# Optimization experiments

Measured on AMD Instinct MI355X. Metric: run time of the kernel, lower is better.

The kernel has to match this reference:

```python
import jax, jax.numpy as jnp
import numpy as np

N_NODES = 50000
N_EDGES = 300000
HEADS = 2
OUT_CH = 128
BN_EPS = 1e-5
NEG_SLOPE = 0.2


def _batchnorm(x, g, b):
    # training-mode BatchNorm1d: biased batch statistics
    mean = x.mean(axis=0)
    var = x.var(axis=0)
    return (x - mean) * jax.lax.rsqrt(var + BN_EPS) * g + b


def _gatv2(x, src, dst, edge_attr, Wl, bl, Wr, br, We, att, bias, concat):
    # PyG GATv2Conv, share_weights=False, aggr='add'
    n = x.shape[0]
    xl = (x @ Wl + bl).reshape(n, HEADS, OUT_CH)  # source messages
    xr = (x @ Wr + br).reshape(n, HEADS, OUT_CH)  # destination term
    ee = (edge_attr @ We).reshape(-1, HEADS, OUT_CH)
    s = jax.nn.leaky_relu(xl[src] + xr[dst] + ee, NEG_SLOPE)  # [E,H,C]
    alpha = jnp.einsum('ehc,hc->eh', s, att)  # [E,H]
    # segment softmax over edges grouped by destination node
    m = jax.ops.segment_max(alpha, dst, num_segments=n)
    a = jnp.exp(alpha - m[dst])
    den = jax.ops.segment_sum(a, dst, num_segments=n)
    a = a / (den[dst] + 1e-16)
    out = jax.ops.segment_sum(xl[src] * a[:, :, None], dst, num_segments=n)  # [N,H,C]
    out = out.reshape(n, HEADS * OUT_CH) if concat else out.mean(axis=1)
    return out + bias


def setup_inputs() -> dict:
    key = jax.random.key(0)
    ks = jax.random.split(key, 16)
    d = {}
    d['h'] = jax.random.normal(ks[0], (N_NODES, 5), jnp.float32)
    d['edge_index'] = jax.random.randint(ks[1], (2, N_EDGES), 0, N_NODES, jnp.int64)
    d['edge_weight'] = jax.random.uniform(ks[2], (N_EDGES, 1), jnp.float32)
    d['bn0_g'] = jnp.ones((5,), jnp.float32)
    d['bn0_b'] = jnp.zeros((5,), jnp.float32)
    d['bn1_g'] = jnp.ones((256,), jnp.float32)
    d['bn1_b'] = jnp.zeros((256,), jnp.float32)
    def lin(k, fan_in, fan_out):
        return jax.random.normal(k, (fan_in, fan_out), jnp.float32) * (1.0 / np.sqrt(fan_in))
    # conv1: in=5 -> heads*out=256, concat=True
    d['c1_Wl'] = lin(ks[3], 5, 256); d['c1_bl'] = jnp.zeros((256,), jnp.float32)
    d['c1_Wr'] = lin(ks[4], 5, 256); d['c1_br'] = jnp.zeros((256,), jnp.float32)
    d['c1_We'] = lin(ks[5], 1, 256)
    d['c1_att'] = jax.random.normal(ks[6], (HEADS, OUT_CH), jnp.float32) * 0.1
    d['c1_bias'] = jnp.zeros((256,), jnp.float32)
    # mu: in=256 -> 128, concat=False
    d['mu_Wl'] = lin(ks[7], 256, 256); d['mu_bl'] = jnp.zeros((256,), jnp.float32)
    d['mu_Wr'] = lin(ks[8], 256, 256); d['mu_br'] = jnp.zeros((256,), jnp.float32)
    d['mu_We'] = lin(ks[9], 1, 256)
    d['mu_att'] = jax.random.normal(ks[10], (HEADS, OUT_CH), jnp.float32) * 0.1
    d['mu_bias'] = jnp.zeros((128,), jnp.float32)
    # log_std: same shapes as mu
    d['ls_Wl'] = lin(ks[11], 256, 256); d['ls_bl'] = jnp.zeros((256,), jnp.float32)
    d['ls_Wr'] = lin(ks[12], 256, 256); d['ls_br'] = jnp.zeros((256,), jnp.float32)
    d['ls_We'] = lin(ks[13], 1, 256)
    d['ls_att'] = jax.random.normal(ks[14], (HEADS, OUT_CH), jnp.float32) * 0.1
    d['ls_bias'] = jnp.zeros((128,), jnp.float32)
    return d


def reference(h, edge_index, edge_weight, bn0_g, bn0_b, bn1_g, bn1_b,
              c1_Wl, c1_bl, c1_Wr, c1_br, c1_We, c1_att, c1_bias,
              mu_Wl, mu_bl, mu_Wr, mu_br, mu_We, mu_att, mu_bias,
              ls_Wl, ls_bl, ls_Wr, ls_br, ls_We, ls_att, ls_bias):
    src, dst = edge_index[0], edge_index[1]
    x = _batchnorm(h, bn0_g, bn0_b)
    x = _gatv2(x, src, dst, edge_weight, c1_Wl, c1_bl, c1_Wr, c1_br, c1_We, c1_att, c1_bias, concat=True)
    x = jax.nn.relu(_batchnorm(x, bn1_g, bn1_b))
    # dropout identity (eval / deterministic)
    mu = _gatv2(x, src, dst, edge_weight, mu_Wl, mu_bl, mu_Wr, mu_br, mu_We, mu_att, mu_bias, concat=False)
    log_std = _gatv2(x, src, dst, edge_weight, ls_Wl, ls_bl, ls_Wr, ls_br, ls_We, ls_att, ls_bias, concat=False)
    return (mu, log_std)
```

## Files before the change

### kernel.cpp

```cpp
#include <hip/hip_runtime.h>
#include <math.h>

#define N_NODES 50000
#define N_EDGES 300000
#define BN_EPS 1e-5f
#define NEG_SLOPE 0.2f

#define RB_COUNT 3128
#define SCAN_TILES 49
#define BN1_BLOCKS 523

typedef short bf8v __attribute__((ext_vector_type(8)));
typedef float f4v __attribute__((ext_vector_type(4)));
typedef float f2v __attribute__((ext_vector_type(2)));

__device__ inline unsigned short f2bf(float f) {
    union { float f; unsigned u; } c; c.f = f;
    unsigned r = c.u + 0x7fffu + ((c.u >> 16) & 1u);
    return (unsigned short)(r >> 16);
}

__device__ inline f2v bfpair(unsigned u) {
    union { unsigned u; float f; } lo, hi;
    lo.u = u << 16;
    hi.u = u & 0xffff0000u;
    f2v r; r.x = lo.f; r.y = hi.f;
    return r;
}

__device__ inline void async_copy16(void* lds, const void* g) {
    __builtin_amdgcn_global_load_lds(
        (const __attribute__((address_space(1))) unsigned int*)g,
        (__attribute__((address_space(3))) unsigned int*)lds, 16, 0, 0);
}

__global__ void bn0_reduce(const float* __restrict__ h, float* __restrict__ acc ) {
    __shared__ float lds[4][10];
    int tid = threadIdx.x;
    int lane = tid & 63, wave = tid >> 6;
    float ls[5] = {0,0,0,0,0}, lq[5] = {0,0,0,0,0};
    for (int r = blockIdx.x * 256 + tid; r < N_NODES; r += 128 * 256) {
        #pragma unroll
        for (int k = 0; k < 5; k++) {
            float v = h[r*5 + k];
            ls[k] += v; lq[k] += v*v;
        }
    }
    #pragma unroll
    for (int k = 0; k < 5; k++) {
        #pragma unroll
        for (int m = 1; m <= 32; m <<= 1) {
            ls[k] += __shfl_xor(ls[k], m, 64);
            lq[k] += __shfl_xor(lq[k], m, 64);
        }
    }
    if (lane == 0) {
        #pragma unroll
        for (int k = 0; k < 5; k++) { lds[wave][k] = ls[k]; lds[wave][5+k] = lq[k]; }
    }
    __syncthreads();
    if (tid < 10) {
        float s = lds[0][tid] + lds[1][tid] + lds[2][tid] + lds[3][tid];
        atomicAdd(&acc[tid], s);
    }
}

__global__ void bn0_finalize(const float* __restrict__ acc, const float* __restrict__ g,
                             const float* __restrict__ b, float* __restrict__ ss) {
    int tid = threadIdx.x;
    if (tid < 5) {
        float mean = acc[tid] * (1.f / N_NODES);
        float var  = acc[5 + tid] * (1.f / N_NODES) - mean*mean;
        float sc = g[tid] * rsqrtf(var + BN_EPS);
        ss[tid]     = sc;
        ss[5 + tid] = b[tid] - mean * sc;
    }
}

__global__ void edge_count(const int* __restrict__ dst, int* __restrict__ count) {
    int e = blockIdx.x * blockDim.x + threadIdx.x;
    if (e < N_EDGES) atomicAdd(&count[dst[e]], 1);
}

__global__ void local_scan(const int* __restrict__ count, int* __restrict__ offsets,
                           int* __restrict__ tileSum) {
    __shared__ int lds[1024];
    int tid = threadIdx.x;
    int i = blockIdx.x * 1024 + tid;
    int v = (i < N_NODES) ? count[i] : 0;
    lds[tid] = v;
    __syncthreads();
    #pragma unroll
    for (int off = 1; off < 1024; off <<= 1) {
        int t = (tid >= off) ? lds[tid - off] : 0;
        __syncthreads();
        lds[tid] += t;
        __syncthreads();
    }
    if (i < N_NODES) offsets[i] = lds[tid] - v;
    if (tid == 1023) tileSum[blockIdx.x] = lds[1023];
}

__global__ void tile_scan(const int* __restrict__ tileSum, int* __restrict__ tilePrefix,
                          int* __restrict__ offsets) {
    int lane = threadIdx.x;
    int v = (lane < SCAN_TILES) ? tileSum[lane] : 0;
    int inc = v;
    #pragma unroll
    for (int off = 1; off < 64; off <<= 1) {
        int t = __shfl_up(inc, off, 64);
        if (lane >= off) inc += t;
    }
    int excl = inc - v;
    if (lane < SCAN_TILES) tilePrefix[lane] = excl;
    if (lane == SCAN_TILES - 1) offsets[N_NODES] = inc;
}

__global__ void add_prefix(int* __restrict__ offsets, const int* __restrict__ tilePrefix,
                           int* __restrict__ cursor) {
    int i = blockIdx.x * 1024 + threadIdx.x;
    if (i < N_NODES) {
        int o = offsets[i] + tilePrefix[blockIdx.x];
        offsets[i] = o;
        cursor[i] = o;
    }
}

__global__ void edge_scatter(const int* __restrict__ dst, const int* __restrict__ src,
                             const float* __restrict__ ew, int* __restrict__ cursor,
                             int* __restrict__ srcp, float* __restrict__ ewp) {
    int e = blockIdx.x * blockDim.x + threadIdx.x;
    if (e < N_EDGES) {
        int pos = atomicAdd(&cursor[dst[e]], 1);
        srcp[pos] = src[e];
        ewp[pos] = ew[e];
    }
}

__global__ void gemm_k5(const float* __restrict__ h, const float* __restrict__ ss,
                        const float* __restrict__ Wl, const float* __restrict__ bl,
                        const float* __restrict__ Wr, const float* __restrict__ br,
                        unsigned short* __restrict__ xl, unsigned short* __restrict__ xr) {
    int n = blockIdx.x;
    int c = threadIdx.x * 2;
    float a[5];
    #pragma unroll
    for (int k = 0; k < 5; k++) a[k] = h[n*5 + k] * ss[k] + ss[5 + k];
    float l0 = bl[c], l1 = bl[c+1], r0 = br[c], r1 = br[c+1];
    #pragma unroll
    for (int k = 0; k < 5; k++) {
        l0 += a[k] * Wl[k*256 + c];
        l1 += a[k] * Wl[k*256 + c + 1];
        r0 += a[k] * Wr[k*256 + c];
        r1 += a[k] * Wr[k*256 + c + 1];
    }
    unsigned lp = (unsigned)f2bf(l0) | ((unsigned)f2bf(l1) << 16);
    unsigned rp = (unsigned)f2bf(r0) | ((unsigned)f2bf(r1) << 16);
    *reinterpret_cast<unsigned*>(xl + (size_t)n*256 + c) = lp;
    *reinterpret_cast<unsigned*>(xr + (size_t)n*256 + c) = rp;
}

__global__ void pack_x_bn(const float* __restrict__ x, const float* __restrict__ ss1,
                          unsigned short* __restrict__ ap) {
    int t = blockIdx.x * 256 + threadIdx.x;
    int lane = t & 63;
    int kc = (t >> 6) & 7;
    int rb = t >> 9;
    int row = rb * 16 + (lane & 15);
    int k0 = kc * 32 + (lane >> 4) * 8;
    union { unsigned short h[8]; uint4 u; } tmp;
    if (row < N_NODES) {
        const float* s = x + (size_t)row * 256 + k0;
        #pragma unroll
        for (int j = 0; j < 8; j++) {
            int c = k0 + j;
            float v = s[j] * ss1[c] + ss1[256 + c];
            v = v > 0.f ? v : 0.f;
            tmp.h[j] = f2bf(v);
        }
    } else {
        #pragma unroll
        for (int j = 0; j < 8; j++) tmp.h[j] = 0;
    }
    *reinterpret_cast<uint4*>(ap + (size_t)t * 8) = tmp.u;
}

__global__ void pack_w(const float* __restrict__ Wl0, const float* __restrict__ Wr0,
                       const float* __restrict__ Wl1, const float* __restrict__ Wr1,
                       unsigned short* __restrict__ bp) {
    int t = blockIdx.x * 256 + threadIdx.x;
    int lane = t & 63;
    int nt = (t >> 6) & 31;
    int kc = (t >> 11) & 7;
    int conv = t >> 14;
    int col = nt * 16 + (lane & 15);
    int k0 = kc * 32 + (lane >> 4) * 8;
    const float* W = conv ? (col < 256 ? Wl1 : Wr1) : (col < 256 ? Wl0 : Wr0);
    int c = col & 255;
    union { unsigned short h[8]; uint4 u; } tmp;
    #pragma unroll
    for (int j = 0; j < 8; j++) tmp.h[j] = f2bf(W[(size_t)(k0 + j) * 256 + c]);
    *reinterpret_cast<uint4*>(bp + (size_t)t * 8) = tmp.u;
}

__global__ __launch_bounds__(512) void gemm_mfma(const unsigned short* __restrict__ ap,
        const unsigned short* __restrict__ bp,
        const float* __restrict__ bl, const float* __restrict__ br,
        unsigned short* __restrict__ xl, unsigned short* __restrict__ xr) {
    __shared__ unsigned short Bs[2][32][512];
    int lane = threadIdx.x & 63;
    int wave = threadIdx.x >> 6;
    int h = wave & 1;
    int rb = blockIdx.x * 4 + (wave >> 1);

    const unsigned short* aptr = ap + (size_t)rb * 4096 + lane * 8;
    const unsigned short* bsrc = bp + lane * 8;

    auto stage = [&](int buf, int kc) {
        #pragma unroll
        for (int j = 0; j < 4; j++) {
            int f = wave * 4 + j;
            async_copy16(&Bs[buf][f][lane * 8], bsrc + (size_t)kc * 16384 + f * 512);
        }
    };
    stage(0, 0);

    bf8v a[8];
    #pragma unroll
    for (int kc = 0; kc < 8; kc++) a[kc] = *reinterpret_cast<const bf8v*>(aptr + kc * 512);

    f4v acc[16];
    #pragma unroll
    for (int t = 0; t < 16; t++) acc[t] = (f4v){0.f, 0.f, 0.f, 0.f};

    for (int kc = 0; kc < 8; kc++) {
        __syncthreads();
        if (kc < 7) stage((kc + 1) & 1, kc + 1);
        const unsigned short* bb = &Bs[kc & 1][h * 16][lane * 8];
        #pragma unroll
        for (int t = 0; t < 16; t++) {
            bf8v b = *reinterpret_cast<const bf8v*>(bb + t * 512);
            acc[t] = __builtin_amdgcn_mfma_f32_16x16x32_bf16(a[kc], b, acc[t], 0, 0, 0);
        }
    }

    int c15 = lane & 15;
    int row0 = rb * 16 + (lane >> 4) * 4;
    unsigned short* outp = h ? xr : xl;
    const float* bias = h ? br : bl;
    #pragma unroll
    for (int t = 0; t < 16; t++) {
        int col = t * 16 + c15;
        float bv = bias[col];
        #pragma unroll
        for (int r = 0; r < 4; r++) {
            int row = row0 + r;
            if (row < N_NODES) outp[(size_t)row * 256 + col] = f2bf(acc[t][r] + bv);
        }
    }
}

__global__ __launch_bounds__(256) void agg_concat(
        const unsigned short* __restrict__ xl, const unsigned short* __restrict__ xr,
        const float* __restrict__ We, const float* __restrict__ att,
        const int* __restrict__ offsets, const int* __restrict__ srcp,
        const float* __restrict__ ewp, const float* __restrict__ bias,
        float* __restrict__ out) {
    int n = blockIdx.x * 4 + (threadIdx.x >> 6);
    int lane = threadIdx.x & 63;
    int half = lane >> 5;
    int sub  = lane & 31;
    int cb   = (sub >> 4) * 128 + (sub & 15) * 8;
    f2v wv[4], av[4], rv[4];
    {
        f4v t0 = *(const f4v*)(We + cb);
        f4v t1 = *(const f4v*)(We + cb + 4);
        wv[0] = (f2v){t0.x, t0.y}; wv[1] = (f2v){t0.z, t0.w};
        wv[2] = (f2v){t1.x, t1.y}; wv[3] = (f2v){t1.z, t1.w};
        t0 = *(const f4v*)(att + cb);
        t1 = *(const f4v*)(att + cb + 4);
        av[0] = (f2v){t0.x, t0.y}; av[1] = (f2v){t0.z, t0.w};
        av[2] = (f2v){t1.x, t1.y}; av[3] = (f2v){t1.z, t1.w};
        uint4 r8 = *(const uint4*)(xr + ((size_t)n << 8) + cb);
        rv[0] = bfpair(r8.x); rv[1] = bfpair(r8.y);
        rv[2] = bfpair(r8.z); rv[3] = bfpair(r8.w);
    }
    int beg = offsets[n], end = offsets[n + 1];
    float mrun = -1e30f, den = 0.f;
    f2v acc[4];
    #pragma unroll
    for (int j = 0; j < 4; j++) acc[j] = (f2v){0.f, 0.f};

    int i = beg + half;
    int sN = 0; float wN = 0.f;
    uint4 lN = {0u, 0u, 0u, 0u};
    if (i < end) {
        sN = srcp[i]; wN = ewp[i];
        lN = *(const uint4*)(xl + ((size_t)sN << 8) + cb);
    }
    for (; i < end; i += 2) {
        uint4 l8 = lN; float w = wN;
        int nx = i + 2;
        if (nx < end) {
            sN = srcp[nx]; wN = ewp[nx];
            lN = *(const uint4*)(xl + ((size_t)sN << 8) + cb);
        }
        f2v w2 = (f2v){w, w};
        f2v lv[4];
        lv[0] = bfpair(l8.x); lv[1] = bfpair(l8.y);
        lv[2] = bfpair(l8.z); lv[3] = bfpair(l8.w);
        f2v da = (f2v){0.f, 0.f};
        #pragma unroll
        for (int j = 0; j < 4; j++) {
            f2v v = lv[j] + rv[j] + w2 * wv[j];
            f2v s = v * (f2v){NEG_SLOPE, NEG_SLOPE};
            v.x = fmaxf(v.x, s.x); v.y = fmaxf(v.y, s.y);
            da += v * av[j];
        }
        float a = da.x + da.y;
        a += __shfl_xor(a, 1, 64);
        a += __shfl_xor(a, 2, 64);
        a += __shfl_xor(a, 4, 64);
        a += __shfl_xor(a, 8, 64);
        float nm = fmaxf(mrun, a);
        float scl = __expf(mrun - nm);
        float p = __expf(a - nm);
        den = den * scl + p;
        f2v sc2 = (f2v){scl, scl}, p2 = (f2v){p, p};
        #pragma unroll
        for (int j = 0; j < 4; j++) acc[j] = acc[j] * sc2 + p2 * lv[j];
        mrun = nm;
    }
    {
        float mo  = __shfl_xor(mrun, 32, 64);
        float dno = __shfl_xor(den, 32, 64);
        float nm = fmaxf(mrun, mo);
        float s0 = __expf(mrun - nm);
        float s1 = __expf(mo - nm);
        den = den * s0 + dno * s1;
        f2v s02 = (f2v){s0, s0}, s12 = (f2v){s1, s1};
        #pragma unroll
        for (int j = 0; j < 4; j++) {
            f2v ao;
            ao.x = __shfl_xor(acc[j].x, 32, 64);
            ao.y = __shfl_xor(acc[j].y, 32, 64);
            acc[j] = acc[j] * s02 + ao * s12;
        }
    }
    float inv = 1.f / (den + 1e-16f);
    if (lane < 32) {
        float o[8];
        #pragma unroll
        for (int j = 0; j < 4; j++) {
            o[2*j]   = acc[j].x * inv + bias[cb + 2*j];
            o[2*j+1] = acc[j].y * inv + bias[cb + 2*j + 1];
        }
        *(float4*)(out + (size_t)n * 256 + cb)     = *(float4*)&o[0];
        *(float4*)(out + (size_t)n * 256 + cb + 4) = *(float4*)&o[4];
    }
}

__global__ __launch_bounds__(256) void agg_dual(
        const unsigned short* __restrict__ xlA, const unsigned short* __restrict__ xrA,
        const unsigned short* __restrict__ xlB, const unsigned short* __restrict__ xrB,
        const float* __restrict__ WeA, const float* __restrict__ attA,
        const float* __restrict__ WeB, const float* __restrict__ attB,
        const int* __restrict__ offsets, const int* __restrict__ srcp,
        const float* __restrict__ ewp,
        const float* __restrict__ biasA, const float* __restrict__ biasB,
        float* __restrict__ outA, float* __restrict__ outB) {
    int n = blockIdx.x * 4 + (threadIdx.x >> 6);
    int lane = threadIdx.x & 63;
    int half = lane >> 5;
    int sub  = lane & 31;
    int cb   = (sub >> 4) * 128 + (sub & 15) * 8;
    f2v wvA[4], avA[4], rvA[4], wvB[4], avB[4], rvB[4];
    {
        f4v t0 = *(const f4v*)(WeA + cb);
        f4v t1 = *(const f4v*)(WeA + cb + 4);
        wvA[0] = (f2v){t0.x, t0.y}; wvA[1] = (f2v){t0.z, t0.w};
        wvA[2] = (f2v){t1.x, t1.y}; wvA[3] = (f2v){t1.z, t1.w};
        t0 = *(const f4v*)(attA + cb);
        t1 = *(const f4v*)(attA + cb + 4);
        avA[0] = (f2v){t0.x, t0.y}; avA[1] = (f2v){t0.z, t0.w};
        avA[2] = (f2v){t1.x, t1.y}; avA[3] = (f2v){t1.z, t1.w};
        t0 = *(const f4v*)(WeB + cb);
        t1 = *(const f4v*)(WeB + cb + 4);
        wvB[0] = (f2v){t0.x, t0.y}; wvB[1] = (f2v){t0.z, t0.w};
        wvB[2] = (f2v){t1.x, t1.y}; wvB[3] = (f2v){t1.z, t1.w};
        t0 = *(const f4v*)(attB + cb);
        t1 = *(const f4v*)(attB + cb + 4);
        avB[0] = (f2v){t0.x, t0.y}; avB[1] = (f2v){t0.z, t0.w};
        avB[2] = (f2v){t1.x, t1.y}; avB[3] = (f2v){t1.z, t1.w};
        uint4 r8 = *(const uint4*)(xrA + ((size_t)n << 8) + cb);
        rvA[0] = bfpair(r8.x); rvA[1] = bfpair(r8.y);
        rvA[2] = bfpair(r8.z); rvA[3] = bfpair(r8.w);
        r8 = *(const uint4*)(xrB + ((size_t)n << 8) + cb);
        rvB[0] = bfpair(r8.x); rvB[1] = bfpair(r8.y);
        rvB[2] = bfpair(r8.z); rvB[3] = bfpair(r8.w);
    }
    int beg = offsets[n], end = offsets[n + 1];
    float mA = -1e30f, dA = 0.f, mB = -1e30f, dB = 0.f;
    f2v accA[4], accB[4];
    #pragma unroll
    for (int j = 0; j < 4; j++) { accA[j] = (f2v){0.f, 0.f}; accB[j] = (f2v){0.f, 0.f}; }

    int i = beg + half;
    int sN = 0; float wN = 0.f;
    uint4 lNA = {0u, 0u, 0u, 0u}, lNB = {0u, 0u, 0u, 0u};
    if (i < end) {
        sN = srcp[i]; wN = ewp[i];
        size_t o = ((size_t)sN << 8) + cb;
        lNA = *(const uint4*)(xlA + o);
        lNB = *(const uint4*)(xlB + o);
    }
    for (; i < end; i += 2) {
        uint4 lA = lNA, lB = lNB; float w = wN;
        int nx = i + 2;
        if (nx < end) {
            sN = srcp[nx]; wN = ewp[nx];
            size_t o = ((size_t)sN << 8) + cb;
            lNA = *(const uint4*)(xlA + o);
            lNB = *(const uint4*)(xlB + o);
        }
        f2v w2 = (f2v){w, w};
        f2v lvA[4], lvB[4];
        lvA[0] = bfpair(lA.x); lvA[1] = bfpair(lA.y);
        lvA[2] = bfpair(lA.z); lvA[3] = bfpair(lA.w);
        lvB[0] = bfpair(lB.x); lvB[1] = bfpair(lB.y);
        lvB[2] = bfpair(lB.z); lvB[3] = bfpair(lB.w);
        f2v daA = (f2v){0.f, 0.f}, daB = (f2v){0.f, 0.f};
        #pragma unroll
        for (int j = 0; j < 4; j++) {
            f2v vA = lvA[j] + rvA[j] + w2 * wvA[j];
            f2v sA = vA * (f2v){NEG_SLOPE, NEG_SLOPE};
            vA.x = fmaxf(vA.x, sA.x); vA.y = fmaxf(vA.y, sA.y);
            daA += vA * avA[j];
            f2v vB = lvB[j] + rvB[j] + w2 * wvB[j];
            f2v sB = vB * (f2v){NEG_SLOPE, NEG_SLOPE};
            vB.x = fmaxf(vB.x, sB.x); vB.y = fmaxf(vB.y, sB.y);
            daB += vB * avB[j];
        }
        float aA = daA.x + daA.y, aB = daB.x + daB.y;
        float tA, tB;
        tA = __shfl_xor(aA, 1, 64); tB = __shfl_xor(aB, 1, 64); aA += tA; aB += tB;
        tA = __shfl_xor(aA, 2, 64); tB = __shfl_xor(aB, 2, 64); aA += tA; aB += tB;
        tA = __shfl_xor(aA, 4, 64); tB = __shfl_xor(aB, 4, 64); aA += tA; aB += tB;
        tA = __shfl_xor(aA, 8, 64); tB = __shfl_xor(aB, 8, 64); aA += tA; aB += tB;
        float nmA = fmaxf(mA, aA), nmB = fmaxf(mB, aB);
        float sclA = __expf(mA - nmA), pA = __expf(aA - nmA);
        float sclB = __expf(mB - nmB), pB = __expf(aB - nmB);
        dA = dA * sclA + pA;
        dB = dB * sclB + pB;
        f2v scA = (f2v){sclA, sclA}, pA2 = (f2v){pA, pA};
        f2v scB = (f2v){sclB, sclB}, pB2 = (f2v){pB, pB};
        #pragma unroll
        for (int j = 0; j < 4; j++) {
            accA[j] = accA[j] * scA + pA2 * lvA[j];
            accB[j] = accB[j] * scB + pB2 * lvB[j];
        }
        mA = nmA; mB = nmB;
    }
    {
        float mo  = __shfl_xor(mA, 32, 64);
        float dno = __shfl_xor(dA, 32, 64);
        float nm = fmaxf(mA, mo);
        float s0 = __expf(mA - nm);
        float s1 = __expf(mo - nm);
        dA = dA * s0 + dno * s1;
        f2v s02 = (f2v){s0, s0}, s12 = (f2v){s1, s1};
        #pragma unroll
        for (int j = 0; j < 4; j++) {
            f2v ao;
            ao.x = __shfl_xor(accA[j].x, 32, 64);
            ao.y = __shfl_xor(accA[j].y, 32, 64);
            accA[j] = accA[j] * s02 + ao * s12;
        }
    }
    {
        float mo  = __shfl_xor(mB, 32, 64);
        float dno = __shfl_xor(dB, 32, 64);
        float nm = fmaxf(mB, mo);
        float s0 = __expf(mB - nm);
        float s1 = __expf(mo - nm);
        dB = dB * s0 + dno * s1;
        f2v s02 = (f2v){s0, s0}, s12 = (f2v){s1, s1};
        #pragma unroll
        for (int j = 0; j < 4; j++) {
            f2v ao;
            ao.x = __shfl_xor(accB[j].x, 32, 64);
            ao.y = __shfl_xor(accB[j].y, 32, 64);
            accB[j] = accB[j] * s02 + ao * s12;
        }
    }
    float invA = 1.f / (dA + 1e-16f);
    float invB = 1.f / (dB + 1e-16f);
    float oA[8], oB[8], poA[8], poB[8];
    #pragma unroll
    for (int j = 0; j < 4; j++) {
        oA[2*j]   = accA[j].x * invA;
        oA[2*j+1] = accA[j].y * invA;
        oB[2*j]   = accB[j].x * invB;
        oB[2*j+1] = accB[j].y * invB;
    }
    #pragma unroll
    for (int j = 0; j < 8; j++) {
        poA[j] = __shfl_xor(oA[j], 16, 64);
        poB[j] = __shfl_xor(oB[j], 16, 64);
    }
    int q = lane >> 4;
    int c0 = (lane & 15) * 8;
    if (q == 0) {
        float r[8];
        #pragma unroll
        for (int j = 0; j < 8; j++) r[j] = (oA[j] + poA[j]) * 0.5f + biasA[c0 + j];
        *(float4*)(outA + (size_t)n * 128 + c0)     = *(float4*)&r[0];
        *(float4*)(outA + (size_t)n * 128 + c0 + 4) = *(float4*)&r[4];
    } else if (q == 2) {
        float r[8];
        #pragma unroll
        for (int j = 0; j < 8; j++) r[j] = (oB[j] + poB[j]) * 0.5f + biasB[c0 + j];
        *(float4*)(outB + (size_t)n * 128 + c0)     = *(float4*)&r[0];
        *(float4*)(outB + (size_t)n * 128 + c0 + 4) = *(float4*)&r[4];
    }
}

__global__ void bn1_reduce(const float* __restrict__ x, float* __restrict__ part) {
    __shared__ float lds[256][9];
    int tid = threadIdx.x;
    int cg = tid & 63;
    int ph = tid >> 6;
    int r0 = blockIdx.x * 96;
    float s[4] = {0,0,0,0}, q[4] = {0,0,0,0};
    #pragma unroll
    for (int it = 0; it < 24; it++) {
        int row = r0 + it * 4 + ph;
        if (row < N_NODES) {
            float4 v = *(const float4*)(x + (size_t)row * 256 + cg * 4);
            s[0] += v.x; s[1] += v.y; s[2] += v.z; s[3] += v.w;
            q[0] += v.x*v.x; q[1] += v.y*v.y; q[2] += v.z*v.z; q[3] += v.w*v.w;
        }
    }
    #pragma unroll
    for (int j = 0; j < 4; j++) { lds[tid][j] = s[j]; lds[tid][4+j] = q[j]; }
    __syncthreads();
    if (tid < 64) {
        float4 sv, qv;
        float* svp = (float*)&sv; float* qvp = (float*)&qv;
        #pragma unroll
        for (int j = 0; j < 4; j++) {
            svp[j] = lds[tid][j] + lds[tid+64][j] + lds[tid+128][j] + lds[tid+192][j];
            qvp[j] = lds[tid][4+j] + lds[tid+64][4+j] + lds[tid+128][4+j] + lds[tid+192][4+j];
        }
        *(float4*)(part + (size_t)blockIdx.x * 512 + cg * 4) = sv;
        *(float4*)(part + (size_t)blockIdx.x * 512 + 256 + cg * 4) = qv;
    }
}

__global__ void bn1_finalize(const float* __restrict__ part, const float* __restrict__ g,
                             const float* __restrict__ b, float* __restrict__ ss1) {
    __shared__ float lds[8][64];
    int t = threadIdx.x;
    int c = blockIdx.x * 32 + (t & 31);
    int ph = t >> 5;
    float s = 0.f, q = 0.f;
    for (int bi = ph; bi < BN1_BLOCKS; bi += 8) {
        s += part[(size_t)bi * 512 + c];
        q += part[(size_t)bi * 512 + 256 + c];
    }
    lds[ph][t & 31] = s;
    lds[ph][32 + (t & 31)] = q;
    __syncthreads();
    if (t < 32) {
        float ss = 0.f, qq = 0.f;
        #pragma unroll
        for (int p = 0; p < 8; p++) { ss += lds[p][t]; qq += lds[p][32 + t]; }
        float mean = ss * (1.f / N_NODES);
        float var  = qq * (1.f / N_NODES) - mean * mean;
        float sc = g[c] * rsqrtf(var + BN_EPS);
        ss1[c] = sc;
        ss1[256 + c] = b[c] - mean * sc;
    }
}

extern "C" void kernel_launch(void* const* d_in, const int* in_sizes, int n_in,
                              void* d_out, int out_size, void* d_ws, size_t ws_size,
                              hipStream_t stream) {
    const float* h          = (const float*)d_in[0];
    const int*   edge_index = (const int*)d_in[1];
    const int*   src = edge_index;
    const int*   dst = edge_index + N_EDGES;
    const float* ew   = (const float*)d_in[2];
    const float* bn0g = (const float*)d_in[3];
    const float* bn0b = (const float*)d_in[4];
    const float* bn1g = (const float*)d_in[5];
    const float* bn1b = (const float*)d_in[6];
    const float* c1_Wl = (const float*)d_in[7];
    const float* c1_bl = (const float*)d_in[8];
    const float* c1_Wr = (const float*)d_in[9];
    const float* c1_br = (const float*)d_in[10];
    const float* c1_We = (const float*)d_in[11];
    const float* c1_att = (const float*)d_in[12];
    const float* c1_bias = (const float*)d_in[13];
    const float* mu_Wl = (const float*)d_in[14];
    const float* mu_bl = (const float*)d_in[15];
    const float* mu_Wr = (const float*)d_in[16];
    const float* mu_br = (const float*)d_in[17];
    const float* mu_We = (const float*)d_in[18];
    const float* mu_att = (const float*)d_in[19];
    const float* mu_bias = (const float*)d_in[20];
    const float* ls_Wl = (const float*)d_in[21];
    const float* ls_bl = (const float*)d_in[22];
    const float* ls_Wr = (const float*)d_in[23];
    const float* ls_br = (const float*)d_in[24];
    const float* ls_We = (const float*)d_in[25];
    const float* ls_att = (const float*)d_in[26];
    const float* ls_bias = (const float*)d_in[27];

    float* out_mu = (float*)d_out;
    float* out_ls = (float*)d_out + (size_t)N_NODES * 128;

    char* ws = (char*)d_ws;
    size_t off = 0;
    auto alloc = [&](size_t bytes) -> void* {
        void* p = ws + off;
        off += (bytes + 255) / 256 * 256;
        return p;
    };
    unsigned short* xl = (unsigned short*)alloc((size_t)N_NODES * 256 * 2);
    unsigned short* xr = (unsigned short*)alloc((size_t)N_NODES * 256 * 2);
    float* xB      = (float*)alloc((size_t)N_NODES * 256 * 4);
    float* bn0acc  = (float*)alloc(10 * 4);
    float* bn0ss   = (float*)alloc(10 * 4);
    float* bn1part = (float*)alloc((size_t)BN1_BLOCKS * 512 * 4);
    float* bn1ss   = (float*)alloc(512 * 4);
    int*   count   = (int*)alloc((size_t)N_NODES * 4);
    int*   offsets = (int*)alloc((size_t)(N_NODES + 1) * 4);
    int*   cursor  = (int*)alloc((size_t)N_NODES * 4);
    int*   srcp    = (int*)alloc((size_t)N_EDGES * 4);
    float* ewp     = (float*)alloc((size_t)N_EDGES * 4);
    int*   tileSum = (int*)alloc((size_t)SCAN_TILES * 4);
    int*   tilePre = (int*)alloc((size_t)SCAN_TILES * 4);
    unsigned short* Apack = (unsigned short*)alloc((size_t)RB_COUNT * 4096 * 2);
    unsigned short* Bpack = (unsigned short*)alloc((size_t)2 * 131072 * 2);

    unsigned short* xl2 = (unsigned short*)xB;
    unsigned short* xr2 = xl2 + (size_t)N_NODES * 256;

    hipMemsetAsync(count, 0, (size_t)N_NODES * 4, stream);
    hipMemsetAsync(bn0acc, 0, 10 * 4, stream);

    bn0_reduce<<<128, 256, 0, stream>>>(h, bn0acc);
    bn0_finalize<<<1, 64, 0, stream>>>(bn0acc, bn0g, bn0b, bn0ss);

    edge_count<<<(N_EDGES + 255) / 256, 256, 0, stream>>>(dst, count);
    local_scan<<<SCAN_TILES, 1024, 0, stream>>>(count, offsets, tileSum);
    tile_scan<<<1, 64, 0, stream>>>(tileSum, tilePre, offsets);
    add_prefix<<<SCAN_TILES, 1024, 0, stream>>>(offsets, tilePre, cursor);
    edge_scatter<<<(N_EDGES + 255) / 256, 256, 0, stream>>>(dst, src, ew, cursor, srcp, ewp);

    pack_w<<<128, 256, 0, stream>>>(mu_Wl, mu_Wr, ls_Wl, ls_Wr, Bpack);

    gemm_k5<<<N_NODES, 128, 0, stream>>>(h, bn0ss, c1_Wl, c1_bl, c1_Wr, c1_br, xl, xr);
    agg_concat<<<N_NODES / 4, 256, 0, stream>>>(xl, xr, c1_We, c1_att, offsets,
                                                srcp, ewp, c1_bias, xB);

    bn1_reduce<<<BN1_BLOCKS, 256, 0, stream>>>(xB, bn1part);
    bn1_finalize<<<8, 256, 0, stream>>>(bn1part, bn1g, bn1b, bn1ss);
    pack_x_bn<<<6256, 256, 0, stream>>>(xB, bn1ss, Apack);

    gemm_mfma<<<782, 512, 0, stream>>>(Apack, Bpack, mu_bl, mu_br, xl, xr);
    gemm_mfma<<<782, 512, 0, stream>>>(Apack, Bpack + 131072, ls_bl, ls_br, xl2, xr2);

    agg_dual<<<N_NODES / 4, 256, 0, stream>>>(xl, xr, xl2, xr2,
                                              mu_We, mu_att, ls_We, ls_att,
                                              offsets, srcp, ewp,
                                              mu_bias, ls_bias, out_mu, out_ls);
}
```

Baseline: 459.3 us.

## Store conv1 output in bf16, fuse small kernels, grid-stride k5 gemm, deeper prefetch

The conv1 aggregation output is now stored as bf16 instead of fp32. This halves the traffic written by agg_concat and read by bn1_reduce and pack_x_bn. The bn0_finalize and tile_scan kernels are folded into gemm_k5 and add_prefix, which removes two tiny launches. gemm_k5 becomes a grid-stride kernel that keeps its weights in registers, and the aggregation loops prefetch source indices two steps ahead. The extra bf16 rounding before batchnorm adds precision risk, and offsets[N_NODES] is now hardcoded to N_EDGES.

```diff
diff --git a/kernel.cpp b/kernel.cpp
--- a/kernel.cpp
+++ b/kernel.cpp
@@ -9,6 +9,7 @@
 #define RB_COUNT 3128
 #define SCAN_TILES 49
 #define BN1_BLOCKS 523
+#define K5_BLOCKS 1024
 
 typedef short bf8v __attribute__((ext_vector_type(8)));
 typedef float f4v __attribute__((ext_vector_type(4)));
@@ -62,18 +63,6 @@
     if (tid < 10) {
         float s = lds[0][tid] + lds[1][tid] + lds[2][tid] + lds[3][tid];
         atomicAdd(&acc[tid], s);
-    }
-}
-
-__global__ void bn0_finalize(const float* __restrict__ acc, const float* __restrict__ g,
-                             const float* __restrict__ b, float* __restrict__ ss) {
-    int tid = threadIdx.x;
-    if (tid < 5) {
-        float mean = acc[tid] * (1.f / N_NODES);
-        float var  = acc[5 + tid] * (1.f / N_NODES) - mean*mean;
-        float sc = g[tid] * rsqrtf(var + BN_EPS);
-        ss[tid]     = sc;
-        ss[5 + tid] = b[tid] - mean * sc;
     }
 }
 
@@ -101,29 +90,24 @@
     if (tid == 1023) tileSum[blockIdx.x] = lds[1023];
 }
 
-__global__ void tile_scan(const int* __restrict__ tileSum, int* __restrict__ tilePrefix,
-                          int* __restrict__ offsets) {
-    int lane = threadIdx.x;
-    int v = (lane < SCAN_TILES) ? tileSum[lane] : 0;
-    int inc = v;
-    #pragma unroll
-    for (int off = 1; off < 64; off <<= 1) {
-        int t = __shfl_up(inc, off, 64);
-        if (lane >= off) inc += t;
-    }
-    int excl = inc - v;
-    if (lane < SCAN_TILES) tilePrefix[lane] = excl;
-    if (lane == SCAN_TILES - 1) offsets[N_NODES] = inc;
-}
-
-__global__ void add_prefix(int* __restrict__ offsets, const int* __restrict__ tilePrefix,
+__global__ void add_prefix(int* __restrict__ offsets, const int* __restrict__ tileSum,
                            int* __restrict__ cursor) {
-    int i = blockIdx.x * 1024 + threadIdx.x;
+    __shared__ int spref;
+    int tid = threadIdx.x;
+    if (tid < 64) {
+        int v = (tid < blockIdx.x) ? tileSum[tid] : 0;
+        #pragma unroll
+        for (int m = 1; m <= 32; m <<= 1) v += __shfl_xor(v, m, 64);
+        if (tid == 0) spref = v;
+    }
+    __syncthreads();
+    int i = blockIdx.x * 1024 + tid;
     if (i < N_NODES) {
-        int o = offsets[i] + tilePrefix[blockIdx.x];
+        int o = offsets[i] + spref;
         offsets[i] = o;
         cursor[i] = o;
     }
+    if (blockIdx.x == 0 && tid == 0) offsets[N_NODES] = N_EDGES;
 }
 
 __global__ void edge_scatter(const int* __restrict__ dst, const int* __restrict__ src,
@@ -137,30 +121,58 @@
     }
 }
 
-__global__ void gemm_k5(const float* __restrict__ h, const float* __restrict__ ss,
-                        const float* __restrict__ Wl, const float* __restrict__ bl,
-                        const float* __restrict__ Wr, const float* __restrict__ br,
-                        unsigned short* __restrict__ xl, unsigned short* __restrict__ xr) {
+__global__ __launch_bounds__(128) void gemm_k5(const float* __restrict__ h,
+        const float* __restrict__ acc10, const float* __restrict__ g5,
+        const float* __restrict__ b5,
+        const float* __restrict__ Wl, const float* __restrict__ bl,
+        const float* __restrict__ Wr, const float* __restrict__ br,
+        unsigned short* __restrict__ xl, unsigned short* __restrict__ xr) {
+    int c = threadIdx.x * 2;
+    float sc[5], sh[5];
+    #pragma unroll
+    for (int k = 0; k < 5; k++) {
+        float mean = acc10[k] * (1.f / N_NODES);
+        float var  = acc10[5 + k] * (1.f / N_NODES) - mean * mean;
+        float s = g5[k] * rsqrtf(var + BN_EPS);
+        sc[k] = s; sh[k] = b5[k] - mean * s;
+    }
+    float wl0[5], wl1[5], wr0[5], wr1[5];
+    #pragma unroll
+    for (int k = 0; k < 5; k++) {
+        wl0[k] = Wl[k*256 + c]; wl1[k] = Wl[k*256 + c + 1];
+        wr0[k] = Wr[k*256 + c]; wr1[k] = Wr[k*256 + c + 1];
+    }
+    float bl0 = bl[c], bl1 = bl[c+1], br0 = br[c], br1 = br[c+1];
     int n = blockIdx.x;
-    int c = threadIdx.x * 2;
-    float a[5];
-    #pragma unroll
-    for (int k = 0; k < 5; k++) a[k] = h[n*5 + k] * ss[k] + ss[5 + k];
-    float l0 = bl[c], l1 = bl[c+1], r0 = br[c], r1 = br[c+1];
-    #pragma unroll
-    for (int k = 0; k < 5; k++) {
-        l0 += a[k] * Wl[k*256 + c];
-        l1 += a[k] * Wl[k*256 + c + 1];
-        r0 += a[k] * Wr[k*256 + c];
-        r1 += a[k] * Wr[k*256 + c + 1];
-    }
-    unsigned lp = (unsigned)f2bf(l0) | ((unsigned)f2bf(l1) << 16);
-    unsigned rp = (unsigned)f2bf(r0) | ((unsigned)f2bf(r1) << 16);
-    *reinterpret_cast<unsigned*>(xl + (size_t)n*256 + c) = lp;
-    *reinterpret_cast<unsigned*>(xr + (size_t)n*256 + c) = rp;
-}
-
-__global__ void pack_x_bn(const float* __restrict__ x, const float* __restrict__ ss1,
+    float hv[5];
+    if (n < N_NODES) {
+        #pragma unroll
+        for (int k = 0; k < 5; k++) hv[k] = h[n*5 + k];
+    }
+    for (; n < N_NODES; n += K5_BLOCKS) {
+        int n2 = n + K5_BLOCKS;
+        float hn[5] = {0,0,0,0,0};
+        if (n2 < N_NODES) {
+            #pragma unroll
+            for (int k = 0; k < 5; k++) hn[k] = h[n2*5 + k];
+        }
+        float l0 = bl0, l1 = bl1, r0 = br0, r1 = br1;
+        #pragma unroll
+        for (int k = 0; k < 5; k++) {
+            float a = hv[k] * sc[k] + sh[k];
+            l0 += a * wl0[k]; l1 += a * wl1[k];
+            r0 += a * wr0[k]; r1 += a * wr1[k];
+        }
+        unsigned lp = (unsigned)f2bf(l0) | ((unsigned)f2bf(l1) << 16);
+        unsigned rp = (unsigned)f2bf(r0) | ((unsigned)f2bf(r1) << 16);
+        *reinterpret_cast<unsigned*>(xl + (size_t)n*256 + c) = lp;
+        *reinterpret_cast<unsigned*>(xr + (size_t)n*256 + c) = rp;
+        #pragma unroll
+        for (int k = 0; k < 5; k++) hv[k] = hn[k];
+    }
+}
+
+__global__ void pack_x_bn(const unsigned short* __restrict__ xh, const float* __restrict__ ss1,
                           unsigned short* __restrict__ ap) {
     int t = blockIdx.x * 256 + threadIdx.x;
     int lane = t & 63;
@@ -170,11 +182,17 @@
     int k0 = kc * 32 + (lane >> 4) * 8;
     union { unsigned short h[8]; uint4 u; } tmp;
     if (row < N_NODES) {
-        const float* s = x + (size_t)row * 256 + k0;
+        uint4 u = *(const uint4*)(xh + (size_t)row * 256 + k0);
+        float f[8];
+        f2v p;
+        p = bfpair(u.x); f[0] = p.x; f[1] = p.y;
+        p = bfpair(u.y); f[2] = p.x; f[3] = p.y;
+        p = bfpair(u.z); f[4] = p.x; f[5] = p.y;
+        p = bfpair(u.w); f[6] = p.x; f[7] = p.y;
         #pragma unroll
         for (int j = 0; j < 8; j++) {
-            int c = k0 + j;
-            float v = s[j] * ss1[c] + ss1[256 + c];
+            int cc = k0 + j;
+            float v = f[j] * ss1[cc] + ss1[256 + cc];
             v = v > 0.f ? v : 0.f;
             tmp.h[j] = f2bf(v);
         }
@@ -265,7 +283,7 @@
         const float* __restrict__ We, const float* __restrict__ att,
         const int* __restrict__ offsets, const int* __restrict__ srcp,
         const float* __restrict__ ewp, const float* __restrict__ bias,
-        float* __restrict__ out) {
+        unsigned short* __restrict__ outh) {
     int n = blockIdx.x * 4 + (threadIdx.x >> 6);
     int lane = threadIdx.x & 63;
     int half = lane >> 5;
@@ -292,19 +310,21 @@
     for (int j = 0; j < 4; j++) acc[j] = (f2v){0.f, 0.f};
 
     int i = beg + half;
-    int sN = 0; float wN = 0.f;
+    float wN = 0.f, wP = 0.f;
+    int sP = 0;
     uint4 lN = {0u, 0u, 0u, 0u};
     if (i < end) {
-        sN = srcp[i]; wN = ewp[i];
-        lN = *(const uint4*)(xl + ((size_t)sN << 8) + cb);
-    }
+        int s0 = srcp[i]; wN = ewp[i];
+        lN = *(const uint4*)(xl + ((size_t)s0 << 8) + cb);
+    }
+    if (i + 2 < end) { sP = srcp[i + 2]; wP = ewp[i + 2]; }
     for (; i < end; i += 2) {
         uint4 l8 = lN; float w = wN;
-        int nx = i + 2;
-        if (nx < end) {
-            sN = srcp[nx]; wN = ewp[nx];
-            lN = *(const uint4*)(xl + ((size_t)sN << 8) + cb);
-        }
+        if (i + 2 < end) {
+            lN = *(const uint4*)(xl + ((size_t)sP << 8) + cb);
+            wN = wP;
+        }
+        if (i + 4 < end) { sP = srcp[i + 4]; wP = ewp[i + 4]; }
         f2v w2 = (f2v){w, w};
         f2v lv[4];
         lv[0] = bfpair(l8.x); lv[1] = bfpair(l8.y);
@@ -349,14 +369,13 @@
     }
     float inv = 1.f / (den + 1e-16f);
     if (lane < 32) {
-        float o[8];
-        #pragma unroll
-        for (int j = 0; j < 4; j++) {
-            o[2*j]   = acc[j].x * inv + bias[cb + 2*j];
-            o[2*j+1] = acc[j].y * inv + bias[cb + 2*j + 1];
-        }
-        *(float4*)(out + (size_t)n * 256 + cb)     = *(float4*)&o[0];
-        *(float4*)(out + (size_t)n * 256 + cb + 4) = *(float4*)&o[4];
+        union { unsigned short hh[8]; uint4 u; } o;
+        #pragma unroll
+        for (int j = 0; j < 4; j++) {
+            o.hh[2*j]   = f2bf(acc[j].x * inv + bias[cb + 2*j]);
+            o.hh[2*j+1] = f2bf(acc[j].y * inv + bias[cb + 2*j + 1]);
+        }
+        *(uint4*)(outh + (size_t)n * 256 + cb) = o.u;
     }
 }
 
@@ -406,23 +425,25 @@
     for (int j = 0; j < 4; j++) { accA[j] = (f2v){0.f, 0.f}; accB[j] = (f2v){0.f, 0.f}; }
 
     int i = beg + half;
-    int sN = 0; float wN = 0.f;
+    float wN = 0.f, wP = 0.f;
+    int sP = 0;
     uint4 lNA = {0u, 0u, 0u, 0u}, lNB = {0u, 0u, 0u, 0u};
     if (i < end) {
-        sN = srcp[i]; wN = ewp[i];
-        size_t o = ((size_t)sN << 8) + cb;
+        int s0 = srcp[i]; wN = ewp[i];
+        size_t o = ((size_t)s0 << 8) + cb;
         lNA = *(const uint4*)(xlA + o);
         lNB = *(const uint4*)(xlB + o);
     }
+    if (i + 2 < end) { sP = srcp[i + 2]; wP = ewp[i + 2]; }
     for (; i < end; i += 2) {
         uint4 lA = lNA, lB = lNB; float w = wN;
-        int nx = i + 2;
-        if (nx < end) {
-            sN = srcp[nx]; wN = ewp[nx];
-            size_t o = ((size_t)sN << 8) + cb;
+        if (i + 2 < end) {
+            size_t o = ((size_t)sP << 8) + cb;
             lNA = *(const uint4*)(xlA + o);
             lNB = *(const uint4*)(xlB + o);
-        }
+            wN = wP;
+        }
+        if (i + 4 < end) { sP = srcp[i + 4]; wP = ewp[i + 4]; }
         f2v w2 = (f2v){w, w};
         f2v lvA[4], lvB[4];
         lvA[0] = bfpair(lA.x); lvA[1] = bfpair(lA.y);
@@ -525,7 +546,7 @@
     }
 }
 
-__global__ void bn1_reduce(const float* __restrict__ x, float* __restrict__ part) {
+__global__ void bn1_reduce(const unsigned short* __restrict__ xh, float* __restrict__ part) {
     __shared__ float lds[256][9];
     int tid = threadIdx.x;
     int cg = tid & 63;
@@ -536,9 +557,10 @@
     for (int it = 0; it < 24; it++) {
         int row = r0 + it * 4 + ph;
         if (row < N_NODES) {
-            float4 v = *(const float4*)(x + (size_t)row * 256 + cg * 4);
-            s[0] += v.x; s[1] += v.y; s[2] += v.z; s[3] += v.w;
-            q[0] += v.x*v.x; q[1] += v.y*v.y; q[2] += v.z*v.z; q[3] += v.w*v.w;
+            uint2 v = *(const uint2*)(xh + (size_t)row * 256 + cg * 4);
+            f2v p0 = bfpair(v.x), p1 = bfpair(v.y);
+            s[0] += p0.x; s[1] += p0.y; s[2] += p1.x; s[3] += p1.y;
+            q[0] += p0.x*p0.x; q[1] += p0.y*p0.y; q[2] += p1.x*p1.x; q[3] += p1.y*p1.y;
         }
     }
     #pragma unroll
@@ -629,9 +651,9 @@
     };
     unsigned short* xl = (unsigned short*)alloc((size_t)N_NODES * 256 * 2);
     unsigned short* xr = (unsigned short*)alloc((size_t)N_NODES * 256 * 2);
-    float* xB      = (float*)alloc((size_t)N_NODES * 256 * 4);
+    unsigned short* xBh = (unsigned short*)alloc((size_t)N_NODES * 256 * 2);
+    unsigned short* xr2 = (unsigned short*)alloc((size_t)N_NODES * 256 * 2);
     float* bn0acc  = (float*)alloc(10 * 4);
-    float* bn0ss   = (float*)alloc(10 * 4);
     float* bn1part = (float*)alloc((size_t)BN1_BLOCKS * 512 * 4);
     float* bn1ss   = (float*)alloc(512 * 4);
     int*   count   = (int*)alloc((size_t)N_NODES * 4);
@@ -640,34 +662,31 @@
     int*   srcp    = (int*)alloc((size_t)N_EDGES * 4);
     float* ewp     = (float*)alloc((size_t)N_EDGES * 4);
     int*   tileSum = (int*)alloc((size_t)SCAN_TILES * 4);
-    int*   tilePre = (int*)alloc((size_t)SCAN_TILES * 4);
     unsigned short* Apack = (unsigned short*)alloc((size_t)RB_COUNT * 4096 * 2);
     unsigned short* Bpack = (unsigned short*)alloc((size_t)2 * 131072 * 2);
 
-    unsigned short* xl2 = (unsigned short*)xB;
-    unsigned short* xr2 = xl2 + (size_t)N_NODES * 256;
+    unsigned short* xl2 = xBh;
 
     hipMemsetAsync(count, 0, (size_t)N_NODES * 4, stream);
     hipMemsetAsync(bn0acc, 0, 10 * 4, stream);
 
     bn0_reduce<<<128, 256, 0, stream>>>(h, bn0acc);
-    bn0_finalize<<<1, 64, 0, stream>>>(bn0acc, bn0g, bn0b, bn0ss);
 
     edge_count<<<(N_EDGES + 255) / 256, 256, 0, stream>>>(dst, count);
     local_scan<<<SCAN_TILES, 1024, 0, stream>>>(count, offsets, tileSum);
-    tile_scan<<<1, 64, 0, stream>>>(tileSum, tilePre, offsets);
-    add_prefix<<<SCAN_TILES, 1024, 0, stream>>>(offsets, tilePre, cursor);
+    add_prefix<<<SCAN_TILES, 1024, 0, stream>>>(offsets, tileSum, cursor);
     edge_scatter<<<(N_EDGES + 255) / 256, 256, 0, stream>>>(dst, src, ew, cursor, srcp, ewp);
 
     pack_w<<<128, 256, 0, stream>>>(mu_Wl, mu_Wr, ls_Wl, ls_Wr, Bpack);
 
-    gemm_k5<<<N_NODES, 128, 0, stream>>>(h, bn0ss, c1_Wl, c1_bl, c1_Wr, c1_br, xl, xr);
+    gemm_k5<<<K5_BLOCKS, 128, 0, stream>>>(h, bn0acc, bn0g, bn0b,
+                                           c1_Wl, c1_bl, c1_Wr, c1_br, xl, xr);
     agg_concat<<<N_NODES / 4, 256, 0, stream>>>(xl, xr, c1_We, c1_att, offsets,
-                                                srcp, ewp, c1_bias, xB);
-
-    bn1_reduce<<<BN1_BLOCKS, 256, 0, stream>>>(xB, bn1part);
+                                                srcp, ewp, c1_bias, xBh);
+
+    bn1_reduce<<<BN1_BLOCKS, 256, 0, stream>>>(xBh, bn1part);
     bn1_finalize<<<8, 256, 0, stream>>>(bn1part, bn1g, bn1b, bn1ss);
-    pack_x_bn<<<6256, 256, 0, stream>>>(xB, bn1ss, Apack);
+    pack_x_bn<<<6256, 256, 0, stream>>>(xBh, bn1ss, Apack);
 
     gemm_mfma<<<782, 512, 0, stream>>>(Apack, Bpack, mu_bl, mu_br, xl, xr);
     gemm_mfma<<<782, 512, 0, stream>>>(Apack, Bpack + 131072, ls_bl, ls_br, xl2, xr2);
```

Measured after the change: 419.4 us. 1.1x faster.
